# Kernel optimization log

Measured on AMD Instinct MI355X. Metric: run time of the kernel, lower is better.

## Reference

```python
import jax, jax.numpy as jnp
import numpy as np

N_NODES = 100000
N_EDGES = 1600000
D_IN = 128
D_OUT = 128


def setup_inputs() -> dict:
    key = jax.random.key(0)
    k1, k2, k3, k4, k5 = jax.random.split(key, 5)
    x = jax.random.normal(k1, (N_NODES, D_IN), dtype=jnp.float32)
    # glorot_init: uniform in [-r, r], r = sqrt(6/(n_in+n_out))
    r = np.sqrt(6.0 / (D_IN + D_OUT))
    weight = jax.random.uniform(k2, (D_IN, D_OUT), dtype=jnp.float32, minval=-r, maxval=r)
    edge_vals = jax.random.uniform(k3, (N_EDGES,), dtype=jnp.float32)
    edge_rows = jax.random.randint(k4, (N_EDGES,), 0, N_NODES, dtype=jnp.int32)
    edge_cols = jax.random.randint(k5, (N_EDGES,), 0, N_NODES, dtype=jnp.int32)
    return {"x": x, "weight": weight, "edge_vals": edge_vals,
            "edge_rows": edge_rows, "edge_cols": edge_cols}


def reference(x, weight, edge_vals, edge_rows, edge_cols):
    # h = x @ W   [N, d_out]
    h = jnp.matmul(x, weight)
    # spmm: out[r] = sum_{edges e with row r} val_e * h[col_e]
    msg = edge_vals[:, None] * h[edge_cols]          # [E, d_out] gather
    agg = jax.ops.segment_sum(msg, edge_rows, num_segments=N_NODES)  # scatter-add
    return jax.nn.relu(agg)
```

## Files before the change

kernel.cpp:

```cpp
#include <hip/hip_runtime.h>
#include <hip/hip_bf16.h>

#define N_NODES 100000
#define N_EDGES 1600000
#define D 128
#define N_TILES 6250
#define NB 512
#define RPB 196
#define BCAP 3584
#define SA_EDGES 3125
#define CAP 16

typedef __bf16 bf16x8 __attribute__((ext_vector_type(8)));
typedef float  f32x4  __attribute__((ext_vector_type(4)));
typedef float  f32x2  __attribute__((ext_vector_type(2)));
typedef int    i32x2  __attribute__((ext_vector_type(2)));

__global__ __launch_bounds__(256) void prep_kernel(const float* __restrict__ W,
                                                   __bf16* __restrict__ WT,
                                                   int* __restrict__ bucketCnt) {
    int t = blockIdx.x * 256 + threadIdx.x;
    int k = t >> 7, n = t & 127;
    WT[n * D + k] = (__bf16)W[t];
    if (t < NB) bucketCnt[t] = 0;
}

__global__ __launch_bounds__(256) void gemm_kernel(
        const float* __restrict__ x,
        const __bf16* __restrict__ WT,
        __bf16* __restrict__ h) {
    __shared__ __bf16 lsm[4][16][144];
    const int wave = threadIdx.x >> 6;
    const int lane = threadIdx.x & 63;
    const int tile = blockIdx.x * 4 + wave;
    if (tile >= N_TILES) return;
    const int m = lane & 15, quad = lane >> 4;
    const float* xp = x + (size_t)(tile * 16 + m) * D + quad * 8;

    f32x4 acc[8];
#pragma unroll
    for (int ct = 0; ct < 8; ++ct) acc[ct] = (f32x4)(0.0f);
#pragma unroll
    for (int kk = 0; kk < 4; ++kk) {
        f32x4 a0 = *(const f32x4*)(xp + kk * 32);
        f32x4 a1 = *(const f32x4*)(xp + kk * 32 + 4);
        bf16x8 a;
#pragma unroll
        for (int j = 0; j < 4; ++j) { a[j] = (__bf16)a0[j]; a[j + 4] = (__bf16)a1[j]; }
#pragma unroll
        for (int ct = 0; ct < 8; ++ct) {
            bf16x8 b = *(const bf16x8*)(WT + (size_t)(ct * 16 + m) * D + kk * 32 + quad * 8);
            acc[ct] = __builtin_amdgcn_mfma_f32_16x16x32_bf16(a, b, acc[ct], 0, 0, 0);
        }
    }
#pragma unroll
    for (int ct = 0; ct < 8; ++ct)
#pragma unroll
        for (int r = 0; r < 4; ++r)
            lsm[wave][quad * 4 + r][ct * 16 + m] = (__bf16)acc[ct][r];
#pragma unroll
    for (int i = 0; i < 4; ++i) {
        int rl = i * 4 + quad;
        bf16x8 vv = *(const bf16x8*)&lsm[wave][rl][m * 8];
        *(bf16x8*)(h + (size_t)(tile * 16 + rl) * D + m * 8) = vv;
    }
}

__global__ __launch_bounds__(256) void scatterA_kernel(
        const int* __restrict__ rows, const int* __restrict__ cols,
        const float* __restrict__ vals,
        int* __restrict__ bucketCnt, i32x2* __restrict__ svcA) {
    __shared__ i32x2 buf[NB][CAP];
    __shared__ int   cnt[NB];
    for (int t = threadIdx.x; t < NB; t += 256) cnt[t] = 0;
    __syncthreads();
    const int base = blockIdx.x * SA_EDGES;
    for (int it = 0; it < 13; ++it) {
        int idx = it * 256 + threadIdx.x;
        if (idx < SA_EDGES) {
            int e = base + idx;
            int r = rows[e];
            int b = r / RPB;
            int local = r - b * RPB;
            i32x2 pk;
            pk[0] = (local << 17) | cols[e];
            pk[1] = __float_as_int(vals[e]);
            int p = atomicAdd(&cnt[b], 1);
            if (p < CAP) buf[b][p] = pk;
            else {
                int g = atomicAdd(&bucketCnt[b], 1);
                if (g < BCAP) svcA[(size_t)b * BCAP + g] = pk;
            }
        }
    }
    __syncthreads();
    for (int t = threadIdx.x; t < NB; t += 256) {
        int n = min(cnt[t], CAP);
        if (n > 0) {
            int g = atomicAdd(&bucketCnt[t], n);
            i32x2* dst = svcA + (size_t)t * BCAP;
            for (int i = 0; i < n; ++i)
                if (g + i < BCAP) dst[g + i] = buf[t][i];
        }
    }
}

__global__ __launch_bounds__(1024) void sortsum_kernel(
        const __bf16* __restrict__ h, const int* __restrict__ bucketCnt,
        const i32x2* __restrict__ svcA, float* __restrict__ out) {
    __shared__ i32x2 lbuf[BCAP];
    __shared__ int   lhist[256];
    __shared__ int   send[256];
    __shared__ int   lcur[256];
    const int b   = blockIdx.x;
    const int tid = threadIdx.x;
    const int n   = min(bucketCnt[b], BCAP);
    const i32x2* win = svcA + (size_t)b * BCAP;

    if (tid < 256) lhist[tid] = 0;
    __syncthreads();

    i32x2 rec0, rec1, rec2, rec3;
    const int i0 = tid, i1 = tid + 1024, i2 = tid + 2048, i3 = tid + 3072;
    if (i0 < n) { rec0 = win[i0]; atomicAdd(&lhist[((unsigned)rec0[0]) >> 17], 1); }
    if (i1 < n) { rec1 = win[i1]; atomicAdd(&lhist[((unsigned)rec1[0]) >> 17], 1); }
    if (i2 < n) { rec2 = win[i2]; atomicAdd(&lhist[((unsigned)rec2[0]) >> 17], 1); }
    if (i3 < n) { rec3 = win[i3]; atomicAdd(&lhist[((unsigned)rec3[0]) >> 17], 1); }
    __syncthreads();

    int v = 0;
    if (tid < 256) { v = lhist[tid]; send[tid] = v; }
    __syncthreads();
    for (int d = 1; d < 256; d <<= 1) {
        int t2 = 0;
        if (tid < 256 && tid >= d) t2 = send[tid - d];
        __syncthreads();
        if (tid < 256) send[tid] += t2;
        __syncthreads();
    }
    if (tid < 256) lcur[tid] = send[tid] - v;
    __syncthreads();

    if (i0 < n) { int rl = ((unsigned)rec0[0]) >> 17; lbuf[atomicAdd(&lcur[rl], 1)] = rec0; }
    if (i1 < n) { int rl = ((unsigned)rec1[0]) >> 17; lbuf[atomicAdd(&lcur[rl], 1)] = rec1; }
    if (i2 < n) { int rl = ((unsigned)rec2[0]) >> 17; lbuf[atomicAdd(&lcur[rl], 1)] = rec2; }
    if (i3 < n) { int rl = ((unsigned)rec3[0]) >> 17; lbuf[atomicAdd(&lcur[rl], 1)] = rec3; }
    __syncthreads();

    const int wave = tid >> 6;
    const int lane = tid & 63;
    for (int rl = wave; rl < RPB; rl += 16) {
        int gr = b * RPB + rl;
        if (gr >= N_NODES) break;
        int s = rl ? send[rl - 1] : 0;
        int e = send[rl];

        float a0 = 0.f, b0 = 0.f, a1 = 0.f, b1 = 0.f;
        float a2 = 0.f, b2 = 0.f, a3 = 0.f, b3 = 0.f;
        int i = s;
        for (; i + 3 < e; i += 4) {
            i32x2 e0 = lbuf[i], e1 = lbuf[i + 1], e2 = lbuf[i + 2], e3 = lbuf[i + 3];
            unsigned u0 = *((const unsigned*)(h + (size_t)(e0[0] & 0x1FFFF) * D) + lane);
            unsigned u1 = *((const unsigned*)(h + (size_t)(e1[0] & 0x1FFFF) * D) + lane);
            unsigned u2 = *((const unsigned*)(h + (size_t)(e2[0] & 0x1FFFF) * D) + lane);
            unsigned u3 = *((const unsigned*)(h + (size_t)(e3[0] & 0x1FFFF) * D) + lane);
            float v0 = __int_as_float(e0[1]), v1 = __int_as_float(e1[1]);
            float v2 = __int_as_float(e2[1]), v3 = __int_as_float(e3[1]);
            a0 += v0 * __int_as_float(u0 << 16);  b0 += v0 * __int_as_float(u0 & 0xffff0000u);
            a1 += v1 * __int_as_float(u1 << 16);  b1 += v1 * __int_as_float(u1 & 0xffff0000u);
            a2 += v2 * __int_as_float(u2 << 16);  b2 += v2 * __int_as_float(u2 & 0xffff0000u);
            a3 += v3 * __int_as_float(u3 << 16);  b3 += v3 * __int_as_float(u3 & 0xffff0000u);
        }
        for (; i < e; ++i) {
            i32x2 e0 = lbuf[i];
            unsigned u0 = *((const unsigned*)(h + (size_t)(e0[0] & 0x1FFFF) * D) + lane);
            float v0 = __int_as_float(e0[1]);
            a0 += v0 * __int_as_float(u0 << 16);  b0 += v0 * __int_as_float(u0 & 0xffff0000u);
        }

        f32x2 o;
        o[0] = fmaxf((a0 + a1) + (a2 + a3), 0.0f);
        o[1] = fmaxf((b0 + b1) + (b2 + b3), 0.0f);
        __builtin_nontemporal_store(o, (f32x2*)(out + (size_t)gr * D + lane * 2));
    }
}

extern "C" void kernel_launch(void* const* d_in, const int* in_sizes, int n_in,
                              void* d_out, int out_size, void* d_ws, size_t ws_size,
                              hipStream_t stream) {
    const float* x    = (const float*)d_in[0];
    const float* w    = (const float*)d_in[1];
    const float* vals = (const float*)d_in[2];
    const int*   rows = (const int*)d_in[3];
    const int*   cols = (const int*)d_in[4];
    float*       out  = (float*)d_out;

    char* p = (char*)d_ws;
    __bf16* h         = (__bf16*)p;  p += (size_t)N_NODES * D * 2;
    __bf16* WT        = (__bf16*)p;  p += (size_t)D * D * 2;
    int*    bucketCnt = (int*)p;     p += 4096;
    i32x2*  svcA      = (i32x2*)p;   p += (size_t)NB * BCAP * 8;

    prep_kernel<<<64, 256, 0, stream>>>(w, WT, bucketCnt);
    gemm_kernel<<<(N_TILES + 3) / 4, 256, 0, stream>>>(x, WT, h);
    scatterA_kernel<<<NB, 256, 0, stream>>>(rows, cols, vals, bucketCnt, svcA);
    sortsum_kernel<<<NB, 1024, 0, stream>>>(h, bucketCnt, svcA, out);
}
```

Baseline: 232.2 us.

## Sort bucket edges by column chunk then row to improve gather locality

The sortsum kernel now sorts each bucket's edges by a composite key of column-range chunk (bits 13-16 of the column) and local row, instead of by local row only. All waves then sweep the chunks in the same order, so gathers of h rows across a block and across concurrently running blocks hit a narrower column range at a time, which is meant to improve L2/MALL reuse. The row-sum loop now keeps per-row accumulators in registers across chunks, and the 256-entry scan is replaced by a 64-lane shuffle scan over 2560 keys. In exchange it adds a larger LDS histogram, more register pressure (13 f32x2 accumulators), more serial loop iterations with short segments, and a single-wave scan.

```diff
diff --git a/kernel.cpp b/kernel.cpp
--- a/kernel.cpp
+++ b/kernel.cpp
@@ -10,6 +10,9 @@
 #define BCAP 3584
 #define SA_EDGES 3125
 #define CAP 16
+#define NCH 13
+#define KEYS 2548
+#define KEYP 2560
 
 typedef __bf16 bf16x8 __attribute__((ext_vector_type(8)));
 typedef float  f32x4  __attribute__((ext_vector_type(4)));
@@ -105,83 +108,114 @@
     }
 }
 
-__global__ __launch_bounds__(1024) void sortsum_kernel(
+__device__ __forceinline__ f32x2 bf2f(unsigned u) {
+    f32x2 r;
+    r[0] = __int_as_float(u << 16);
+    r[1] = __int_as_float(u & 0xffff0000u);
+    return r;
+}
+
+__device__ __forceinline__ int sortkey(unsigned u) {
+    return (int)((u >> 13) & 15u) * RPB + (int)(u >> 17);
+}
+
+__global__ __launch_bounds__(1024, 8) void sortsum_kernel(
         const __bf16* __restrict__ h, const int* __restrict__ bucketCnt,
         const i32x2* __restrict__ svcA, float* __restrict__ out) {
     __shared__ i32x2 lbuf[BCAP];
-    __shared__ int   lhist[256];
-    __shared__ int   send[256];
-    __shared__ int   lcur[256];
+    __shared__ int   lhist[KEYP];
+    __shared__ int   send[KEYP];
+    __shared__ int   lcur[KEYP];
     const int b   = blockIdx.x;
     const int tid = threadIdx.x;
     const int n   = min(bucketCnt[b], BCAP);
     const i32x2* win = svcA + (size_t)b * BCAP;
 
-    if (tid < 256) lhist[tid] = 0;
+    for (int t = tid; t < KEYP; t += 1024) lhist[t] = 0;
     __syncthreads();
 
     i32x2 rec0, rec1, rec2, rec3;
     const int i0 = tid, i1 = tid + 1024, i2 = tid + 2048, i3 = tid + 3072;
-    if (i0 < n) { rec0 = win[i0]; atomicAdd(&lhist[((unsigned)rec0[0]) >> 17], 1); }
-    if (i1 < n) { rec1 = win[i1]; atomicAdd(&lhist[((unsigned)rec1[0]) >> 17], 1); }
-    if (i2 < n) { rec2 = win[i2]; atomicAdd(&lhist[((unsigned)rec2[0]) >> 17], 1); }
-    if (i3 < n) { rec3 = win[i3]; atomicAdd(&lhist[((unsigned)rec3[0]) >> 17], 1); }
-    __syncthreads();
-
-    int v = 0;
-    if (tid < 256) { v = lhist[tid]; send[tid] = v; }
-    __syncthreads();
-    for (int d = 1; d < 256; d <<= 1) {
-        int t2 = 0;
-        if (tid < 256 && tid >= d) t2 = send[tid - d];
-        __syncthreads();
-        if (tid < 256) send[tid] += t2;
-        __syncthreads();
-    }
-    if (tid < 256) lcur[tid] = send[tid] - v;
-    __syncthreads();
-
-    if (i0 < n) { int rl = ((unsigned)rec0[0]) >> 17; lbuf[atomicAdd(&lcur[rl], 1)] = rec0; }
-    if (i1 < n) { int rl = ((unsigned)rec1[0]) >> 17; lbuf[atomicAdd(&lcur[rl], 1)] = rec1; }
-    if (i2 < n) { int rl = ((unsigned)rec2[0]) >> 17; lbuf[atomicAdd(&lcur[rl], 1)] = rec2; }
-    if (i3 < n) { int rl = ((unsigned)rec3[0]) >> 17; lbuf[atomicAdd(&lcur[rl], 1)] = rec3; }
+    if (i0 < n) { rec0 = win[i0]; atomicAdd(&lhist[sortkey((unsigned)rec0[0])], 1); }
+    if (i1 < n) { rec1 = win[i1]; atomicAdd(&lhist[sortkey((unsigned)rec1[0])], 1); }
+    if (i2 < n) { rec2 = win[i2]; atomicAdd(&lhist[sortkey((unsigned)rec2[0])], 1); }
+    if (i3 < n) { rec3 = win[i3]; atomicAdd(&lhist[sortkey((unsigned)rec3[0])], 1); }
+    __syncthreads();
+
+    if (tid < 64) {
+        const int base = tid * 40;
+        int run = 0;
+#pragma unroll
+        for (int j = 0; j < 40; ++j) run += lhist[base + j];
+        int s = run;
+#pragma unroll
+        for (int d = 1; d < 64; d <<= 1) {
+            int t2 = __shfl_up(s, d, 64);
+            if (tid >= d) s += t2;
+        }
+        int acc = s - run;
+#pragma unroll
+        for (int j = 0; j < 40; ++j) {
+            int hv = lhist[base + j];
+            lcur[base + j] = acc;
+            acc += hv;
+            send[base + j] = acc;
+        }
+    }
+    __syncthreads();
+
+    if (i0 < n) { lbuf[atomicAdd(&lcur[sortkey((unsigned)rec0[0])], 1)] = rec0; }
+    if (i1 < n) { lbuf[atomicAdd(&lcur[sortkey((unsigned)rec1[0])], 1)] = rec1; }
+    if (i2 < n) { lbuf[atomicAdd(&lcur[sortkey((unsigned)rec2[0])], 1)] = rec2; }
+    if (i3 < n) { lbuf[atomicAdd(&lcur[sortkey((unsigned)rec3[0])], 1)] = rec3; }
     __syncthreads();
 
     const int wave = tid >> 6;
     const int lane = tid & 63;
-    for (int rl = wave; rl < RPB; rl += 16) {
-        int gr = b * RPB + rl;
-        if (gr >= N_NODES) break;
-        int s = rl ? send[rl - 1] : 0;
-        int e = send[rl];
-
-        float a0 = 0.f, b0 = 0.f, a1 = 0.f, b1 = 0.f;
-        float a2 = 0.f, b2 = 0.f, a3 = 0.f, b3 = 0.f;
-        int i = s;
-        for (; i + 3 < e; i += 4) {
-            i32x2 e0 = lbuf[i], e1 = lbuf[i + 1], e2 = lbuf[i + 2], e3 = lbuf[i + 3];
-            unsigned u0 = *((const unsigned*)(h + (size_t)(e0[0] & 0x1FFFF) * D) + lane);
-            unsigned u1 = *((const unsigned*)(h + (size_t)(e1[0] & 0x1FFFF) * D) + lane);
-            unsigned u2 = *((const unsigned*)(h + (size_t)(e2[0] & 0x1FFFF) * D) + lane);
-            unsigned u3 = *((const unsigned*)(h + (size_t)(e3[0] & 0x1FFFF) * D) + lane);
-            float v0 = __int_as_float(e0[1]), v1 = __int_as_float(e1[1]);
-            float v2 = __int_as_float(e2[1]), v3 = __int_as_float(e3[1]);
-            a0 += v0 * __int_as_float(u0 << 16);  b0 += v0 * __int_as_float(u0 & 0xffff0000u);
-            a1 += v1 * __int_as_float(u1 << 16);  b1 += v1 * __int_as_float(u1 & 0xffff0000u);
-            a2 += v2 * __int_as_float(u2 << 16);  b2 += v2 * __int_as_float(u2 & 0xffff0000u);
-            a3 += v3 * __int_as_float(u3 << 16);  b3 += v3 * __int_as_float(u3 & 0xffff0000u);
-        }
-        for (; i < e; ++i) {
-            i32x2 e0 = lbuf[i];
-            unsigned u0 = *((const unsigned*)(h + (size_t)(e0[0] & 0x1FFFF) * D) + lane);
-            float v0 = __int_as_float(e0[1]);
-            a0 += v0 * __int_as_float(u0 << 16);  b0 += v0 * __int_as_float(u0 & 0xffff0000u);
-        }
-
-        f32x2 o;
-        o[0] = fmaxf((a0 + a1) + (a2 + a3), 0.0f);
-        o[1] = fmaxf((b0 + b1) + (b2 + b3), 0.0f);
-        __builtin_nontemporal_store(o, (f32x2*)(out + (size_t)gr * D + lane * 2));
+    const char* hb = (const char*)h;
+    const unsigned lo4 = (unsigned)lane * 4u;
+
+    f32x2 acc[13];
+#pragma unroll
+    for (int r8 = 0; r8 < 13; ++r8) acc[r8] = (f32x2)(0.0f);
+
+    for (int c = 0; c < NCH; ++c) {
+        const int kb = c * RPB;
+#pragma unroll
+        for (int r8 = 0; r8 < 13; ++r8) {
+            const int rl = wave + (r8 << 4);
+            if (rl < RPB) {
+                const int k = kb + rl;
+                int i = (k == 0) ? 0 : send[k - 1];
+                const int e = send[k];
+                f32x2 a = acc[r8];
+                for (; i + 1 < e; i += 2) {
+                    i32x2 q0 = lbuf[i], q1 = lbuf[i + 1];
+                    unsigned u0 = *(const unsigned*)(hb + ((((unsigned)q0[0]) & 0x1FFFFu) << 8) + lo4);
+                    unsigned u1 = *(const unsigned*)(hb + ((((unsigned)q1[0]) & 0x1FFFFu) << 8) + lo4);
+                    a += bf2f(u0) * __int_as_float(q0[1]);
+                    a += bf2f(u1) * __int_as_float(q1[1]);
+                }
+                if (i < e) {
+                    i32x2 q0 = lbuf[i];
+                    unsigned u0 = *(const unsigned*)(hb + ((((unsigned)q0[0]) & 0x1FFFFu) << 8) + lo4);
+                    a += bf2f(u0) * __int_as_float(q0[1]);
+                }
+                acc[r8] = a;
+            }
+        }
+    }
+
+#pragma unroll
+    for (int r8 = 0; r8 < 13; ++r8) {
+        const int rl = wave + (r8 << 4);
+        const int gr = b * RPB + rl;
+        if (rl < RPB && gr < N_NODES) {
+            f32x2 o;
+            o[0] = fmaxf(acc[r8][0], 0.0f);
+            o[1] = fmaxf(acc[r8][1], 0.0f);
+            __builtin_nontemporal_store(o, (f32x2*)(out + (size_t)gr * D + lane * 2));
+        }
     }
 }
 
```

Result: slower. 254.4 us (+9.6%).
